# Performance work log

Measured on AMD Instinct MI355X. Metric: run time of the kernel, lower is better.

The kernel has to match this reference:

```python
import jax, jax.numpy as jnp
import numpy as np


def _depthwise3x3(x_nhwc, w):
    # w: (3, 3, 1, C) — depthwise conv, padding=1, matches torch Conv2d(groups=C)
    return jax.lax.conv_general_dilated(
        x_nhwc, w, window_strides=(1, 1), padding='SAME',
        dimension_numbers=('NHWC', 'HWIO', 'NHWC'),
        feature_group_count=x_nhwc.shape[-1])


def _stripe_attn(q, k, v, lepe_w, B, H, W, nh, hd, ss, axis, scale):
    # q/k/v: (B, H, W, nh*hd); axis 0 = horizontal stripes, 1 = vertical
    pad_h = (-H) % ss if axis == 0 else 0
    pad_w = (-W) % ss if axis == 1 else 0
    if pad_h or pad_w:
        pad = ((0, 0), (0, pad_h), (0, pad_w), (0, 0))
        q, k, v = jnp.pad(q, pad), jnp.pad(k, pad), jnp.pad(v, pad)
    Hp, Wp = q.shape[1], q.shape[2]
    lepe = _depthwise3x3(v, lepe_w)  # (B, Hp, Wp, nh*hd)

    if axis == 0:
        nS = Hp // ss
        def to_win(t):  # -> (B*nS*Wp, nh, ss, hd)
            t = t.reshape(B, nS, ss, Wp, nh, hd)
            return t.transpose(0, 1, 3, 4, 2, 5).reshape(B * nS * Wp, nh, ss, hd)
    else:
        nS = Wp // ss
        def to_win(t):  # -> (B*Hp*nS, nh, ss, hd)
            t = t.reshape(B, Hp, nS, ss, nh, hd)
            return t.transpose(0, 1, 2, 4, 3, 5).reshape(B * Hp * nS, nh, ss, hd)

    qw, kw, vw, lw = to_win(q), to_win(k), to_win(v), to_win(lepe)
    attn = jax.nn.softmax(jnp.einsum('wnqd,wnkd->wnqk', qw, kw) / scale, axis=-1)
    out = jnp.einsum('wnqk,wnkd->wnqd', attn, vw) + lw  # (Wnum, nh, ss, hd)

    if axis == 0:
        out = out.transpose(0, 2, 1, 3).reshape(B, nS, Wp, ss, nh * hd)
        out = out.transpose(0, 1, 3, 2, 4).reshape(B, Hp, Wp, nh * hd)
    else:
        out = out.transpose(0, 2, 1, 3).reshape(B, Hp, nS, ss, nh * hd)
        out = out.reshape(B, Hp, Wp, nh * hd)
    return out[:, :H, :W, :].reshape(B, H * W, nh * hd)


def setup_inputs() -> dict:
    key = jax.random.key(0)
    ks = jax.random.split(key, 6)
    B, H, W, dim, n_heads, ss = 8, 64, 64, 512, 16, 8
    half = dim // 2
    x = jax.random.normal(ks[0], (B, H * W, dim), dtype=jnp.float32)
    w_qkv = jax.random.normal(ks[1], (3 * dim, dim), dtype=jnp.float32) * 0.02
    w_proj = jax.random.normal(ks[2], (dim, dim), dtype=jnp.float32) * 0.02
    b_proj = jnp.zeros((dim,), dtype=jnp.float32)
    lepe_h_w = jax.random.normal(ks[3], (3, 3, 1, half), dtype=jnp.float32) * 0.1
    lepe_v_w = jax.random.normal(ks[4], (3, 3, 1, half), dtype=jnp.float32) * 0.1
    return {"x": x, "w_qkv": w_qkv, "w_proj": w_proj, "b_proj": b_proj,
            "lepe_h_w": lepe_h_w, "lepe_v_w": lepe_v_w, "H": H, "W": W}


def reference(x, w_qkv, w_proj, b_proj, lepe_h_w, lepe_v_w, H, W):
    B, L, C = x.shape
    n_heads, ss = 16, 8
    hd = C // n_heads
    scale = float(np.sqrt(hd))
    qkv = x @ w_qkv.T  # (B, L, 3C)
    q, k, v = jnp.split(qkv, 3, axis=-1)
    q = q.reshape(B, H, W, C)
    k = k.reshape(B, H, W, C)
    v = v.reshape(B, H, W, C)
    half = C // 2
    nh_h = n_heads // 2
    nh_v = n_heads - nh_h
    out_h = _stripe_attn(q[..., :half], k[..., :half], v[..., :half],
                         lepe_h_w, B, H, W, nh_h, hd, ss, axis=0, scale=scale)
    out_v = _stripe_attn(q[..., half:], k[..., half:], v[..., half:],
                         lepe_v_w, B, H, W, nh_v, hd, ss, axis=1, scale=scale)
    out = jnp.concatenate([out_h, out_v], axis=-1)
    return out @ w_proj.T + b_proj
```

## Files before the change

kernel.cpp:

```cpp
#include <hip/hip_runtime.h>
#include <hip/hip_bf16.h>
#include <stdint.h>

typedef _Float16 half2v __attribute__((ext_vector_type(2)));
typedef _Float16 half8v __attribute__((ext_vector_type(8)));
typedef uint32_t u32x4  __attribute__((ext_vector_type(4)));
typedef float    f32x4  __attribute__((ext_vector_type(4)));

__device__ __forceinline__ unsigned short f2h(float f) {
  _Float16 h = (_Float16)f;
  return __builtin_bit_cast(unsigned short, h);
}
__device__ __forceinline__ half2v bch2(uint32_t u) {
  return __builtin_bit_cast(half2v, u);
}

__device__ __forceinline__ int qkv_idx(int half, int b, int n, int h, int w) {
  int idx = half * 8388608 + (b * 8 + n) * 131072;
  idx += (half == 0) ? ((h >> 3) * 16384 + w * 256 + (h & 7) * 32)
                     : (h * 2048 + w * 32);
  return idx;
}

#define GLOAD_LDS16(gsrc, lbase)                                          \
  __builtin_amdgcn_global_load_lds(                                       \
      (const __attribute__((address_space(1))) uint32_t*)(gsrc),          \
      (__attribute__((address_space(3))) uint32_t*)(lbase), 16, 0, 0)

__global__ __launch_bounds__(256) void cvt_f32_f16(const float* __restrict__ in,
                                                   unsigned short* __restrict__ out,
                                                   int n4) {
  int i = blockIdx.x * 256 + threadIdx.x;
  if (i >= n4) return;
  float4 f = reinterpret_cast<const float4*>(in)[i];
  ushort4 u;
  u.x = f2h(f.x); u.y = f2h(f.y); u.z = f2h(f.z); u.w = f2h(f.w);
  reinterpret_cast<ushort4*>(out)[i] = u;
}

template<int MODE>
__global__ __launch_bounds__(256) void gemm_bt(
    const unsigned short* __restrict__ A,
    const unsigned short* __restrict__ B,
    unsigned short* __restrict__ Cq,
    float* __restrict__ Cf,
    const float* __restrict__ bias,
    int M, int N, int K)
{
  __shared__ unsigned short As[128 * 32];
  __shared__ unsigned short Bs[128 * 32];
  const int tid  = threadIdx.x;
  const int m0   = blockIdx.x * 128;
  const int n0   = blockIdx.y * 128;
  const int wave = tid >> 6, lane = tid & 63;
  const int wr = wave >> 1, wc = wave & 1;
  const int sr = tid >> 2;
  const int sc = (tid & 3) * 8;
  const size_t aBase0 = (size_t)(m0 + sr) * K + sc;
  const size_t aBase1 = (size_t)(m0 + 64 + sr) * K + sc;
  const size_t bBase0 = (size_t)(n0 + sr) * K + sc;
  const size_t bBase1 = (size_t)(n0 + 64 + sr) * K + sc;
  char* ldsA = (char*)As + (tid & ~63) * 16;
  char* ldsB = (char*)Bs + (tid & ~63) * 16;

  f32x4 acc[4][4];
  const f32x4 zero = {0.f, 0.f, 0.f, 0.f};
  #pragma unroll
  for (int i = 0; i < 4; ++i)
    #pragma unroll
    for (int j = 0; j < 4; ++j) acc[i][j] = zero;

  const int lr = lane & 15;
  const int lk = (lane >> 4) * 8;

  for (int kt = 0; kt < K; kt += 32) {
    __syncthreads();
    GLOAD_LDS16(A + aBase0 + kt, ldsA);
    GLOAD_LDS16(A + aBase1 + kt, ldsA + 4096);
    GLOAD_LDS16(B + bBase0 + kt, ldsB);
    GLOAD_LDS16(B + bBase1 + kt, ldsB + 4096);
    __syncthreads();
    half8v af[4], bfr[4];
    #pragma unroll
    for (int i = 0; i < 4; ++i)
      af[i] = *reinterpret_cast<const half8v*>(As + (wr * 64 + i * 16 + lr) * 32 + lk);
    #pragma unroll
    for (int j = 0; j < 4; ++j)
      bfr[j] = *reinterpret_cast<const half8v*>(Bs + (wc * 64 + j * 16 + lr) * 32 + lk);
    #pragma unroll
    for (int i = 0; i < 4; ++i)
      #pragma unroll
      for (int j = 0; j < 4; ++j)
        acc[i][j] = __builtin_amdgcn_mfma_f32_16x16x32_f16(af[i], bfr[j], acc[i][j], 0, 0, 0);
  }

  const int cr = (lane >> 4) * 4;
  const int cc = lane & 15;

  if constexpr (MODE == 0) {
    #pragma unroll
    for (int i = 0; i < 4; ++i) {
      #pragma unroll
      for (int j = 0; j < 4; ++j) {
        const int row = m0 + wr * 64 + i * 16 + cr;
        const int col = n0 + wc * 64 + j * 16 + cc;
        #pragma unroll
        for (int t = 0; t < 4; ++t)
          Cf[(size_t)(row + t) * N + col] = acc[i][j][t] + bias[col];
      }
    }
  } else {
    const int mb   = m0 + wr * 64;
    const int btok = mb >> 12;
    const int htok = (mb >> 6) & 63;
    #pragma unroll
    for (int j = 0; j < 4; ++j) {
      const int cb    = n0 + wc * 64 + j * 16;
      const int tq    = cb >> 9;
      const int halfc = (cb >> 8) & 1;
      const int nn    = (cb & 255) >> 5;
      const int ccl   = (cb & 31) + cc;
      const int wstride = halfc ? 32 : 256;
      int base = tq * 16777216 + halfc * 8388608 + (btok * 8 + nn) * 131072 + ccl;
      base += halfc ? (htok * 2048) : ((htok >> 3) * 16384 + (htok & 7) * 32);
      #pragma unroll
      for (int i = 0; i < 4; ++i) {
        #pragma unroll
        for (int t = 0; t < 4; ++t) {
          const int w = i * 16 + cr + t;
          Cq[base + w * wstride] = f2h(acc[i][j][t]);
        }
      }
    }
  }
}

__global__ __launch_bounds__(256) void attn_lepe(
    const unsigned short* __restrict__ qkvp,
    const unsigned short* __restrict__ wlep,
    unsigned short* __restrict__ outp)
{
  const int gw   = (int)((blockIdx.x * 256 + threadIdx.x) >> 6);
  const int lane = threadIdx.x & 63;
  const int half = gw >> 15;
  const int id   = gw & 32767;
  const int b    = id >> 12;
  const int n    = (id >> 9) & 7;
  int h0, w0;
  if (half == 0) { const int s = (id >> 6) & 7; h0 = s * 8; w0 = id & 63; }
  else           { const int s = id & 7; h0 = (id >> 3) & 63; w0 = s * 8; }
  const int winbase = qkv_idx(half, b, n, h0, w0);
  const unsigned short* qwin = qkvp + winbase;
  const unsigned short* kwin = qkvp + 16777216 + winbase;
  const unsigned short* vwin = qkvp + 33554432 + winbase;

  const int qr = lane >> 3, kr = lane & 7;
  const unsigned short* qp = qwin + qr * 32;
  const unsigned short* kp = kwin + kr * 32;
  float s_val = 0.f;
  #pragma unroll
  for (int c = 0; c < 4; ++c) {
    u32x4 qv = *reinterpret_cast<const u32x4*>(qp + c * 8);
    u32x4 kv = *reinterpret_cast<const u32x4*>(kp + c * 8);
    #pragma unroll
    for (int e = 0; e < 4; ++e)
      s_val = __builtin_amdgcn_fdot2(bch2(qv[e]), bch2(kv[e]), s_val, false);
  }
  s_val *= 0.17677669529663687f;

  float p = __expf(s_val);
  float den = p;
  den += __shfl_xor(den, 1);
  den += __shfl_xor(den, 2);
  den += __shfl_xor(den, 4);
  const float a = p * __builtin_amdgcn_rcpf(den);
  const _Float16 ah = (_Float16)a;
  half2v ad = {ah, ah};
  const uint32_t adu = __builtin_bit_cast(uint32_t, ad);

  const int d0 = (lane & 7) * 4;
  const int gb = lane & 56;
  half2v o01 = {0, 0}, o23 = {0, 0};
  #pragma unroll
  for (int k = 0; k < 8; ++k) {
    const half2v ak2 = bch2((uint32_t)__shfl((int)adu, gb | k));
    const uint2 vv = *reinterpret_cast<const uint2*>(vwin + k * 32 + d0);
    o01 += ak2 * bch2(vv.x);
    o23 += ak2 * bch2(vv.y);
  }

  const int hq = h0 + ((half == 0) ? qr : 0);
  const int wq = w0 + ((half == 0) ? 0 : qr);
  const unsigned short* vplane = qkvp + 33554432;
  const unsigned short* wl = wlep + half * 2304 + n * 32 + d0;
  half2v l01 = {0, 0}, l23 = {0, 0};
  #pragma unroll
  for (int dy = -1; dy <= 1; ++dy) {
    #pragma unroll
    for (int dx = -1; dx <= 1; ++dx) {
      const int hh = hq + dy, ww = wq + dx;
      uint2 vv; vv.x = 0u; vv.y = 0u;
      if ((unsigned)hh < 64u && (unsigned)ww < 64u)
        vv = *reinterpret_cast<const uint2*>(vplane + qkv_idx(half, b, n, hh, ww) + d0);
      const uint2 wt = *reinterpret_cast<const uint2*>(wl + ((dy + 1) * 3 + dx + 1) * 256);
      l01 += bch2(wt.x) * bch2(vv.x);
      l23 += bch2(wt.y) * bch2(vv.y);
    }
  }

  const int m = b * 4096 + hq * 64 + wq;
  const int chan0 = half * 256 + n * 32;
  const half2v r01 = o01 + l01;
  const half2v r23 = o23 + l23;
  uint2 r;
  r.x = __builtin_bit_cast(uint32_t, r01);
  r.y = __builtin_bit_cast(uint32_t, r23);
  *reinterpret_cast<uint2*>(outp + (size_t)m * 512 + chan0 + d0) = r;
}

extern "C" void kernel_launch(void* const* d_in, const int* in_sizes, int n_in,
                              void* d_out, int out_size, void* d_ws, size_t ws_size,
                              hipStream_t stream) {
  const float* x      = (const float*)d_in[0];
  const float* w_qkv  = (const float*)d_in[1];
  const float* w_proj = (const float*)d_in[2];
  const float* b_proj = (const float*)d_in[3];
  const float* lepe_h = (const float*)d_in[4];
  const float* lepe_v = (const float*)d_in[5];
  float* out = (float*)d_out;

  char* ws = (char*)d_ws;
  unsigned short* qkv_p   = (unsigned short*)ws;
  unsigned short* xh      = (unsigned short*)(ws + 100663296);
  unsigned short* wqkv_h  = (unsigned short*)(ws + 134217728);
  unsigned short* wproj_h = (unsigned short*)(ws + 135790592);
  unsigned short* wlep_h  = (unsigned short*)(ws + 136314880);

  cvt_f32_f16<<<16384, 256, 0, stream>>>(x, xh, 4194304);
  cvt_f32_f16<<<768,   256, 0, stream>>>(w_qkv, wqkv_h, 196608);
  cvt_f32_f16<<<256,   256, 0, stream>>>(w_proj, wproj_h, 65536);
  cvt_f32_f16<<<3,     256, 0, stream>>>(lepe_h, wlep_h, 576);
  cvt_f32_f16<<<3,     256, 0, stream>>>(lepe_v, wlep_h + 2304, 576);

  gemm_bt<1><<<dim3(256, 12), 256, 0, stream>>>(
      xh, wqkv_h, qkv_p, nullptr, nullptr, 32768, 1536, 512);

  attn_lepe<<<16384, 256, 0, stream>>>(qkv_p, wlep_h, xh);

  gemm_bt<0><<<dim3(256, 4), 256, 0, stream>>>(
      xh, wproj_h, nullptr, out, b_proj, 32768, 512, 512);
}
```

Before: 211.8 us.

## Swizzle GEMM LDS layout and transpose MFMA operands for vectorized epilogue stores

Applies an XOR swizzle to the LDS slot used by the async global-to-LDS loads and to the fragment reads, to reduce LDS bank conflicts. It swaps the MFMA A/B operands so each lane holds four consecutive output columns, which lets the epilogue write float4 rows with a vector bias load, and packed half4 stores via cvt_pkrtz for the QKV layout. The scatter stores become wider and fewer. The f16 conversion changes from round-to-nearest to round-toward-zero, a small change in numerics.

Result: no change. 213.3 us (+0.7%).

```diff
diff --git a/kernel.cpp b/kernel.cpp
--- a/kernel.cpp
+++ b/kernel.cpp
@@ -13,6 +13,9 @@
 }
 __device__ __forceinline__ half2v bch2(uint32_t u) {
   return __builtin_bit_cast(half2v, u);
+}
+__device__ __forceinline__ uint32_t pkrtz_u32(float a, float b) {
+  return __builtin_bit_cast(uint32_t, __builtin_amdgcn_cvt_pkrtz(a, b));
 }
 
 __device__ __forceinline__ int qkv_idx(int half, int b, int n, int h, int w) {
@@ -55,7 +58,7 @@
   const int wave = tid >> 6, lane = tid & 63;
   const int wr = wave >> 1, wc = wave & 1;
   const int sr = tid >> 2;
-  const int sc = (tid & 3) * 8;
+  const int sc = ((tid & 3) ^ ((tid >> 3) & 3)) * 8;
   const size_t aBase0 = (size_t)(m0 + sr) * K + sc;
   const size_t aBase1 = (size_t)(m0 + 64 + sr) * K + sc;
   const size_t bBase0 = (size_t)(n0 + sr) * K + sc;
@@ -70,8 +73,8 @@
     #pragma unroll
     for (int j = 0; j < 4; ++j) acc[i][j] = zero;
 
-  const int lr = lane & 15;
-  const int lk = (lane >> 4) * 8;
+  const int lr   = lane & 15;
+  const int slot = (lane >> 4) ^ ((lr >> 1) & 3);
 
   for (int kt = 0; kt < K; kt += 32) {
     __syncthreads();
@@ -83,15 +86,15 @@
     half8v af[4], bfr[4];
     #pragma unroll
     for (int i = 0; i < 4; ++i)
-      af[i] = *reinterpret_cast<const half8v*>(As + (wr * 64 + i * 16 + lr) * 32 + lk);
+      af[i] = *reinterpret_cast<const half8v*>(As + (wr * 64 + i * 16 + lr) * 32 + slot * 8);
     #pragma unroll
     for (int j = 0; j < 4; ++j)
-      bfr[j] = *reinterpret_cast<const half8v*>(Bs + (wc * 64 + j * 16 + lr) * 32 + lk);
+      bfr[j] = *reinterpret_cast<const half8v*>(Bs + (wc * 64 + j * 16 + lr) * 32 + slot * 8);
     #pragma unroll
     for (int i = 0; i < 4; ++i)
       #pragma unroll
       for (int j = 0; j < 4; ++j)
-        acc[i][j] = __builtin_amdgcn_mfma_f32_16x16x32_f16(af[i], bfr[j], acc[i][j], 0, 0, 0);
+        acc[i][j] = __builtin_amdgcn_mfma_f32_16x16x32_f16(bfr[j], af[i], acc[i][j], 0, 0, 0);
   }
 
   const int cr = (lane >> 4) * 4;
@@ -99,14 +102,18 @@
 
   if constexpr (MODE == 0) {
     #pragma unroll
-    for (int i = 0; i < 4; ++i) {
+    for (int j = 0; j < 4; ++j) {
+      const int n = n0 + wc * 64 + j * 16 + cr;
+      const float4 b4 = *reinterpret_cast<const float4*>(bias + n);
       #pragma unroll
-      for (int j = 0; j < 4; ++j) {
-        const int row = m0 + wr * 64 + i * 16 + cr;
-        const int col = n0 + wc * 64 + j * 16 + cc;
-        #pragma unroll
-        for (int t = 0; t < 4; ++t)
-          Cf[(size_t)(row + t) * N + col] = acc[i][j][t] + bias[col];
+      for (int i = 0; i < 4; ++i) {
+        const int m = m0 + wr * 64 + i * 16 + cc;
+        float4 r;
+        r.x = acc[i][j][0] + b4.x;
+        r.y = acc[i][j][1] + b4.y;
+        r.z = acc[i][j][2] + b4.z;
+        r.w = acc[i][j][3] + b4.w;
+        *reinterpret_cast<float4*>(Cf + (size_t)m * N + n) = r;
       }
     }
   } else {
@@ -115,21 +122,21 @@
     const int htok = (mb >> 6) & 63;
     #pragma unroll
     for (int j = 0; j < 4; ++j) {
-      const int cb    = n0 + wc * 64 + j * 16;
-      const int tq    = cb >> 9;
-      const int halfc = (cb >> 8) & 1;
-      const int nn    = (cb & 255) >> 5;
-      const int ccl   = (cb & 31) + cc;
+      const int nb    = n0 + wc * 64 + j * 16 + cr;
+      const int tq    = nb >> 9;
+      const int halfc = (nb >> 8) & 1;
+      const int nn    = (nb & 255) >> 5;
+      const int ch4   = nb & 31;
+      int base = tq * 16777216 + halfc * 8388608 + (btok * 8 + nn) * 131072 + ch4;
+      base += halfc ? (htok * 2048) : ((htok >> 3) * 16384 + (htok & 7) * 32);
       const int wstride = halfc ? 32 : 256;
-      int base = tq * 16777216 + halfc * 8388608 + (btok * 8 + nn) * 131072 + ccl;
-      base += halfc ? (htok * 2048) : ((htok >> 3) * 16384 + (htok & 7) * 32);
       #pragma unroll
       for (int i = 0; i < 4; ++i) {
-        #pragma unroll
-        for (int t = 0; t < 4; ++t) {
-          const int w = i * 16 + cr + t;
-          Cq[base + w * wstride] = f2h(acc[i][j][t]);
-        }
+        const int wpix = i * 16 + cc;
+        uint2 r;
+        r.x = pkrtz_u32(acc[i][j][0], acc[i][j][1]);
+        r.y = pkrtz_u32(acc[i][j][2], acc[i][j][3]);
+        *reinterpret_cast<uint2*>(Cq + base + wpix * wstride) = r;
       }
     }
   }
```
